# Kernel tuning notes

Measured on AMD Instinct MI355X. Metric: run time of the kernel, lower is better.

Reference implementation:

```python
import jax, jax.numpy as jnp
import numpy as np

LOW_T = 0.05
HIGH_T = 0.15

SOBEL_X = jnp.array([[-1., 0., 1.], [-2., 0., 2.], [-1., 0., 1.]], dtype=jnp.float32).reshape(1, 1, 3, 3)
SOBEL_Y = jnp.array([[1., 2., 1.], [0., 0., 0.], [-1., -2., -1.]], dtype=jnp.float32).reshape(1, 1, 3, 3)


def _conv3x3(x, k):
    # NCHW conv, padding=1, stride=1 (matches F.conv2d(x, k, padding=1))
    return jax.lax.conv_general_dilated(x, k, window_strides=(1, 1), padding=((1, 1), (1, 1)))


def setup_inputs() -> dict:
    key = jax.random.key(0)
    x = jax.random.normal(key, (1, 1, 4096, 4096), dtype=jnp.float32)
    return {"x": x}


def reference(x):
    grad_x = _conv3x3(x, SOBEL_X)
    grad_y = _conv3x3(x, SOBEL_Y)
    grad_mag = jnp.sqrt(grad_x * grad_x + grad_y * grad_y)
    grad_dir = jnp.arctan2(grad_y, grad_x)  # radians, as in the original (compared to degree thresholds)

    m = grad_mag[0, 0]  # [H, W]
    d = grad_dir[0, 0][1:-1, 1:-1]  # direction at interior pixels [H-2, W-2]
    H, W = m.shape

    def sh(dr, dc):
        # magnitude at (row+dr, col+dc) for interior pixels
        return m[1 + dr:H - 1 + dr, 1 + dc:W - 1 + dc]

    mc = sh(0, 0)

    # Branch predicates replicated literally from the torch code (degree thresholds
    # vs radian values; some sub-conditions are vacuously false, kept for faithfulness).
    b1 = ((d >= -22.5) & (d <= 22.5)) | ((d >= 157.5) & (d <= 180.0)) | ((d >= -157.5) & (d <= -180.0))
    b2 = ((d > 22.5) & (d <= 67.5)) | ((d >= -112.5) & (d < -157.5))
    b3 = ((d > 67.5) & (d <= 112.5)) | ((d >= -67.5) & (d < -22.5))

    mag_prev = jnp.where(b1, sh(0, -1), jnp.where(b2, sh(-1, 1), jnp.where(b3, sh(-1, 0), sh(-1, -1))))
    mag_next = jnp.where(b1, sh(0, 1), jnp.where(b2, sh(1, -1), jnp.where(b3, sh(1, 0), sh(1, 1))))

    keep = (mc >= mag_prev) & (mc >= mag_next)
    interior = jnp.where(keep, mc, jnp.zeros_like(mc))
    edges = jnp.zeros_like(m).at[1:-1, 1:-1].set(interior)

    # Double thresholding: strong -> 255, weak ([low, high]) -> 0, below-low passes through.
    strong = edges > HIGH_T
    weak = (edges >= LOW_T) & (edges <= HIGH_T)
    out = jnp.where(strong, jnp.float32(255.0), jnp.where(weak, jnp.float32(0.0), edges))
    return out  # [H, W]
```

## Files before the change

### kernel.cpp

```cpp
#include <hip/hip_runtime.h>
#include <math.h>


constexpr int Wd = 4096;
constexpr int Ht = 4096;

typedef float f4 __attribute__((ext_vector_type(4)));

__global__ __launch_bounds__(256) void canny_kernel(const float* __restrict__ x,
                                                    float* __restrict__ out) {
    const int tid   = threadIdx.x;
    const int strip = blockIdx.x * 64 + (tid & 63);
    const int r     = blockIdx.y * 4  + (tid >> 6);
    const int cbase = strip * 8;

    const int rm = (r == 0) ? 0 : r - 1;
    const int rp = (r == Ht - 1) ? Ht - 1 : r + 1;
    const bool left  = (cbase == 0);
    const bool right = (cbase + 8 == Wd);

    const float* xa = x + (size_t)rm * Wd + (cbase - 4);
    const float* xb = x + (size_t)r  * Wd + (cbase - 4);
    const float* xc = x + (size_t)rp * Wd + (cbase - 4);

    float ar[16], br[16], cr[16];
    const f4 z4 = {0.f, 0.f, 0.f, 0.f};
    #pragma unroll
    for (int k = 0; k < 4; ++k) {
        const bool ok = !((k == 0 && left) || (k == 3 && right));
        f4 va = ok ? *reinterpret_cast<const f4*>(xa + 4 * k) : z4;
        f4 vb = ok ? *reinterpret_cast<const f4*>(xb + 4 * k) : z4;
        f4 vc = ok ? *reinterpret_cast<const f4*>(xc + 4 * k) : z4;
        *reinterpret_cast<f4*>(&ar[4 * k]) = va;
        *reinterpret_cast<f4*>(&br[4 * k]) = vb;
        *reinterpret_cast<f4*>(&cr[4 * k]) = vc;
    }

    float t1[12], t2[12];
    #pragma unroll
    for (int i = 0; i < 12; ++i) {
        float a = ar[i + 2], b = br[i + 2], c = cr[i + 2];
        t1[i] = a + 2.0f * b + c;
        t2[i] = a - c;
    }

    float m[10];
    #pragma unroll
    for (int s = 0; s < 10; ++s) {
        float gx = t1[s + 2] - t1[s];
        float gy = t2[s] + 2.0f * t2[s + 1] + t2[s + 2];
        m[s] = sqrtf(gx * gx + gy * gy);
    }

    float acc[8];
    #pragma unroll
    for (int o = 0; o < 8; ++o) {
        float mc = m[o + 1];
        bool keep = (mc >= m[o]) && (mc >= m[o + 2]);
        float e = keep ? mc : 0.0f;
        acc[o] = (e > 0.15f) ? 255.0f : ((e >= 0.05f) ? 0.0f : e);
    }

    if (r == 0 || r == Ht - 1) {
        #pragma unroll
        for (int o = 0; o < 8; ++o) acc[o] = 0.0f;
    }
    if (left)  acc[0] = 0.0f;
    if (right) acc[7] = 0.0f;

    float* op = out + (size_t)r * Wd + cbase;
    f4 lo = {acc[0], acc[1], acc[2], acc[3]};
    f4 hi = {acc[4], acc[5], acc[6], acc[7]};
    __builtin_nontemporal_store(lo, reinterpret_cast<f4*>(op));
    __builtin_nontemporal_store(hi, reinterpret_cast<f4*>(op) + 1);
}

extern "C" void kernel_launch(void* const* d_in, const int* in_sizes, int n_in,
                              void* d_out, int out_size, void* d_ws, size_t ws_size,
                              hipStream_t stream) {
    const float* x = (const float*)d_in[0];
    float* out = (float*)d_out;
    dim3 grid(Wd / (64 * 8), Ht / 4);
    canny_kernel<<<grid, dim3(256), 0, stream>>>(x, out);
}
```

Baseline: 114.4 us.

## Widen per-thread strip to 16 columns and skip sqrt via squared-magnitude compares

Each thread now handles 16 output columns instead of 8, which cuts the share of redundant halo loads. Non-max suppression and thresholding run on squared magnitudes against squared thresholds, so sqrt is skipped. When values sit near ties or in the pass-through band, a wave-wide hazard check falls back to the exact sqrt path. Stores switch from nontemporal to normal, and edge handling moves to clamped offsets with explicit zeroing.

```diff
diff --git a/kernel.cpp b/kernel.cpp
--- a/kernel.cpp
+++ b/kernel.cpp
@@ -10,69 +10,100 @@
 __global__ __launch_bounds__(256) void canny_kernel(const float* __restrict__ x,
                                                     float* __restrict__ out) {
     const int tid   = threadIdx.x;
-    const int strip = blockIdx.x * 64 + (tid & 63);
-    const int r     = blockIdx.y * 4  + (tid >> 6);
-    const int cbase = strip * 8;
+    const int lane  = tid & 63;
+    const int r     = blockIdx.y * 4 + (tid >> 6);
+    const int cbase = blockIdx.x * 1024 + lane * 16;
 
-    const int rm = (r == 0) ? 0 : r - 1;
-    const int rp = (r == Ht - 1) ? Ht - 1 : r + 1;
-    const bool left  = (cbase == 0);
-    const bool right = (cbase + 8 == Wd);
+    const int rm = r > 0 ? r - 1 : 0;
+    const int rp = r < Ht - 1 ? r + 1 : Ht - 1;
 
-    const float* xa = x + (size_t)rm * Wd + (cbase - 4);
-    const float* xb = x + (size_t)r  * Wd + (cbase - 4);
-    const float* xc = x + (size_t)rp * Wd + (cbase - 4);
+    const float* rowa = x + (size_t)rm * Wd;
+    const float* rowb = x + (size_t)r  * Wd;
+    const float* rowc = x + (size_t)rp * Wd;
 
-    float ar[16], br[16], cr[16];
-    const f4 z4 = {0.f, 0.f, 0.f, 0.f};
+    int off[6];
     #pragma unroll
-    for (int k = 0; k < 4; ++k) {
-        const bool ok = !((k == 0 && left) || (k == 3 && right));
-        f4 va = ok ? *reinterpret_cast<const f4*>(xa + 4 * k) : z4;
-        f4 vb = ok ? *reinterpret_cast<const f4*>(xb + 4 * k) : z4;
-        f4 vc = ok ? *reinterpret_cast<const f4*>(xc + 4 * k) : z4;
-        *reinterpret_cast<f4*>(&ar[4 * k]) = va;
-        *reinterpret_cast<f4*>(&br[4 * k]) = vb;
-        *reinterpret_cast<f4*>(&cr[4 * k]) = vc;
+    for (int k = 0; k < 6; ++k) {
+        int c = cbase - 4 + 4 * k;
+        off[k] = c < 0 ? 0 : (c > Wd - 4 ? Wd - 4 : c);
     }
 
-    float t1[12], t2[12];
+    float ar[24], br[24], cr[24];
     #pragma unroll
-    for (int i = 0; i < 12; ++i) {
-        float a = ar[i + 2], b = br[i + 2], c = cr[i + 2];
-        t1[i] = a + 2.0f * b + c;
-        t2[i] = a - c;
+    for (int k = 0; k < 6; ++k) {
+        *(f4*)(ar + 4 * k) = *(const f4*)(rowa + off[k]);
+        *(f4*)(br + 4 * k) = *(const f4*)(rowb + off[k]);
+        *(f4*)(cr + 4 * k) = *(const f4*)(rowc + off[k]);
     }
 
-    float m[10];
+    float t1[20], t2[20];
     #pragma unroll
-    for (int s = 0; s < 10; ++s) {
-        float gx = t1[s + 2] - t1[s];
-        float gy = t2[s] + 2.0f * t2[s + 1] + t2[s + 2];
-        m[s] = sqrtf(gx * gx + gy * gy);
+    for (int j = 0; j < 20; ++j) {
+        float a = ar[j + 2], b = br[j + 2], c = cr[j + 2];
+        t1[j] = a + 2.0f * b + c;
+        t2[j] = a - c;
     }
 
-    float acc[8];
+    if (blockIdx.x == 0 && lane == 0) {
+        t1[0] = 0.f; t2[0] = 0.f; t1[1] = 0.f; t2[1] = 0.f;
+    }
+    if (blockIdx.x == 3 && lane == 63) {
+        t1[18] = 0.f; t2[18] = 0.f; t1[19] = 0.f; t2[19] = 0.f;
+    }
+
+    float q[18];
     #pragma unroll
-    for (int o = 0; o < 8; ++o) {
-        float mc = m[o + 1];
-        bool keep = (mc >= m[o]) && (mc >= m[o + 2]);
-        float e = keep ? mc : 0.0f;
-        acc[o] = (e > 0.15f) ? 255.0f : ((e >= 0.05f) ? 0.0f : e);
+    for (int i = 0; i < 18; ++i) {
+        float gx = t1[i + 2] - t1[i];
+        float gy = t2[i] + 2.0f * t2[i + 1] + t2[i + 2];
+        q[i] = gx * gx + gy * gy;
+    }
+
+    const float C1  = __uint_as_float(0x3CB851EDu);
+    const float C2B = __uint_as_float(0x3B23D709u);
+
+    bool hazard = false;
+    #pragma unroll
+    for (int i = 0; i < 17; ++i) {
+        int d = (int)(__float_as_uint(q[i + 1]) - __float_as_uint(q[i]));
+        hazard |= ((unsigned)(d + 8) < 17u);
+    }
+
+    float acc[16];
+    #pragma unroll
+    for (int o = 0; o < 16; ++o) {
+        float qp = q[o], qc = q[o + 1], qn = q[o + 2];
+        bool keep = (qc >= qp) && (qc >= qn);
+        acc[o] = (keep && qc > C1) ? 255.0f : 0.0f;
+        hazard |= (keep && qc > 0.0f && qc <= C2B);
+    }
+
+    if (__any(hazard)) {
+        float m[18];
+        #pragma unroll
+        for (int i = 0; i < 18; ++i) m[i] = sqrtf(q[i]);
+        #pragma unroll
+        for (int o = 0; o < 16; ++o) {
+            float mc = m[o + 1];
+            bool keep = (mc >= m[o]) && (mc >= m[o + 2]);
+            float e = keep ? mc : 0.0f;
+            acc[o] = (e > 0.15f) ? 255.0f : ((e >= 0.05f) ? 0.0f : e);
+        }
     }
 
     if (r == 0 || r == Ht - 1) {
         #pragma unroll
-        for (int o = 0; o < 8; ++o) acc[o] = 0.0f;
+        for (int o = 0; o < 16; ++o) acc[o] = 0.0f;
     }
-    if (left)  acc[0] = 0.0f;
-    if (right) acc[7] = 0.0f;
+    if (blockIdx.x == 0 && lane == 0)  acc[0]  = 0.0f;
+    if (blockIdx.x == 3 && lane == 63) acc[15] = 0.0f;
 
     float* op = out + (size_t)r * Wd + cbase;
-    f4 lo = {acc[0], acc[1], acc[2], acc[3]};
-    f4 hi = {acc[4], acc[5], acc[6], acc[7]};
-    __builtin_nontemporal_store(lo, reinterpret_cast<f4*>(op));
-    __builtin_nontemporal_store(hi, reinterpret_cast<f4*>(op) + 1);
+    #pragma unroll
+    for (int k = 0; k < 4; ++k) {
+        f4 v = {acc[4 * k], acc[4 * k + 1], acc[4 * k + 2], acc[4 * k + 3]};
+        *(f4*)(op + 4 * k) = v;
+    }
 }
 
 extern "C" void kernel_launch(void* const* d_in, const int* in_sizes, int n_in,
@@ -80,6 +111,6 @@
                               hipStream_t stream) {
     const float* x = (const float*)d_in[0];
     float* out = (float*)d_out;
-    dim3 grid(Wd / (64 * 8), Ht / 4);
+    dim3 grid(4, 1024);
     canny_kernel<<<grid, dim3(256), 0, stream>>>(x, out);
 }
```

Result: slower. 130.5 us (+14.1%).
